# Kernel tuning notes

Measured on AMD Instinct MI355X. Metric: run time of the kernel, lower is better.

Reference implementation:

```python
import jax, jax.numpy as jnp
import numpy as np

D_MODEL = 1024
N_HEADS = 16
D_K = D_MODEL // N_HEADS


def setup_inputs() -> dict:
    key = jax.random.key(0)
    ks = jax.random.split(key, 9)
    B, S = 2, 2048
    scale = 1.0 / np.sqrt(D_MODEL)
    inp = {
        "X": jax.random.normal(ks[0], (B, S, D_MODEL), dtype=jnp.float32),
        "Wq": jax.random.normal(ks[1], (D_MODEL, D_MODEL), dtype=jnp.float32) * scale,
        "bq": jnp.zeros((D_MODEL,), dtype=jnp.float32),
        "Wk": jax.random.normal(ks[2], (D_MODEL, D_MODEL), dtype=jnp.float32) * scale,
        "bk": jnp.zeros((D_MODEL,), dtype=jnp.float32),
        "Wv": jax.random.normal(ks[3], (D_MODEL, D_MODEL), dtype=jnp.float32) * scale,
        "bv": jnp.zeros((D_MODEL,), dtype=jnp.float32),
        "Wo": jax.random.normal(ks[4], (D_MODEL, D_MODEL), dtype=jnp.float32) * scale,
        "bo": jnp.zeros((D_MODEL,), dtype=jnp.float32),
    }
    return inp


def reference(X, Wq, bq, Wk, bk, Wv, bv, Wo, bo):
    B, S, _ = X.shape
    # QKV projections (torch Linear: x @ W.T + b; here W stored as [in, out])
    Q = X @ Wq + bq
    K = X @ Wk + bk
    V = X @ Wv + bv
    # [B, S, H, Dk] -> [B, H, S, Dk]
    def split_heads(t):
        return t.reshape(B, S, N_HEADS, D_K).transpose(0, 2, 1, 3)
    Q, K, V = split_heads(Q), split_heads(K), split_heads(V)
    scores = jnp.einsum('bhqd,bhkd->bhqk', Q, K) / jnp.sqrt(jnp.float32(D_K))
    attn = jax.nn.softmax(scores, axis=-1)
    out = jnp.einsum('bhqk,bhkd->bhqd', attn, V)  # [B, H, S, Dk]
    out = out.transpose(0, 2, 1, 3).reshape(B, S, D_MODEL)
    return out @ Wo + bo
```

## Files before the change

### kernel.cpp

```cpp
#include <hip/hip_runtime.h>
#include <hip/hip_bf16.h>


typedef __attribute__((ext_vector_type(8))) short short8;
typedef __attribute__((ext_vector_type(4))) float f32x4;
typedef __attribute__((ext_vector_type(2))) float f32x2;
typedef unsigned short u16;
typedef unsigned int u32;

static __device__ __forceinline__ u16 f2bf(float f) {
    union { float f; u32 u; } c; c.f = f;
    u32 u = c.u;
    u32 r = u + 0x7fffu + ((u >> 16) & 1u);
    return (u16)(r >> 16);
}
static __device__ __forceinline__ float bf2f(u16 x) {
    union { u32 u; float f; } c; c.u = ((u32)x) << 16;
    return c.f;
}

#define GL1(p) ((const __attribute__((address_space(1))) void*)(p))
#define LD3(p) ((__attribute__((address_space(3))) void*)(p))
static __device__ __forceinline__ void gld16(const void* g, void* l) {
    __builtin_amdgcn_global_load_lds(GL1(g), LD3(l), 16, 0, 0);
}

#define Q_PRESCALE 0.18033688011112042f

__global__ __launch_bounds__(256) void prep(
    const float* __restrict__ X, u16* __restrict__ Xb,
    const float* __restrict__ Wq, const float* __restrict__ Wk,
    const float* __restrict__ Wv, const float* __restrict__ Wo,
    const float* __restrict__ bq, const float* __restrict__ bk,
    const float* __restrict__ bv,
    u16* __restrict__ Wqkv, u16* __restrict__ Wto, float* __restrict__ Bp)
{
    int id = blockIdx.x;
    int t = threadIdx.x;
    if (id == 5120) {
        for (int i = t; i < 3072; i += 256) {
            int wsel = i >> 10, c = i & 1023;
            float v = (wsel == 0) ? bq[c] * Q_PRESCALE : (wsel == 1 ? bk[c] : bv[c]);
            Bp[i] = v;
        }
        return;
    }
    if (id >= 1024) {
        int i = (id - 1024) * 1024 + t * 4;
        float4 v = *reinterpret_cast<const float4*>(X + i);
        ushort4 o;
        o.x = f2bf(v.x); o.y = f2bf(v.y); o.z = f2bf(v.z); o.w = f2bf(v.w);
        *reinterpret_cast<ushort4*>(Xb + i) = o;
        return;
    }
    int which = id >> 8;
    const float* W; u16* T; float sc;
    switch (which) {
        case 0: W = Wq; T = Wqkv;                sc = Q_PRESCALE; break;
        case 1: W = Wk; T = Wqkv + 1024 * 1024;  sc = 1.0f; break;
        case 2: W = Wv; T = Wqkv + 2048 * 1024;  sc = 1.0f; break;
        default: W = Wo; T = Wto;                sc = 1.0f; break;
    }
    int rem = id & 255;
    int n0 = (rem & 15) * 64, k0 = (rem >> 4) * 64;
    __shared__ float tile[64][65];
    int r = t / 16, c4 = (t % 16) * 4;
    #pragma unroll
    for (int p = 0; p < 4; p++) {
        int row = p * 16 + r;
        float4 v = *reinterpret_cast<const float4*>(W + (k0 + row) * 1024 + n0 + c4);
        tile[row][c4 + 0] = v.x * sc; tile[row][c4 + 1] = v.y * sc;
        tile[row][c4 + 2] = v.z * sc; tile[row][c4 + 3] = v.w * sc;
    }
    __syncthreads();
    #pragma unroll
    for (int p = 0; p < 4; p++) {
        int nrow = p * 16 + r;
        ushort4 o;
        o.x = f2bf(tile[c4 + 0][nrow]); o.y = f2bf(tile[c4 + 1][nrow]);
        o.z = f2bf(tile[c4 + 2][nrow]); o.w = f2bf(tile[c4 + 3][nrow]);
        *reinterpret_cast<ushort4*>(T + (n0 + nrow) * 1024 + k0 + c4) = o;
    }
}

__global__ __launch_bounds__(256, 3) void gemm_qkv(
    const u16* __restrict__ Xb, const u16* __restrict__ Wqkv,
    const float* __restrict__ Bp,
    u16* __restrict__ Qb, u16* __restrict__ Kb, u16* __restrict__ Vtg)
{
    __shared__ __align__(16) u16 As[2][128 * 32];
    __shared__ __align__(16) u16 Bs[2][128 * 32];
    int t = threadIdx.x;
    int w = t >> 6, lane = t & 63, l15 = lane & 15, quad = lane >> 4;
    int wm = (w >> 1) * 64, wn = (w & 1) * 64;
    int bid = blockIdx.x;
    int row0 = (bid & 31) * 128, col0 = (bid >> 5) * 128;

    int drow = lane >> 2;
    int gc8 = ((lane & 3) ^ (drow & 3) ^ ((drow >> 2) & 3)) * 8;
    int asw = ((quad ^ (l15 & 3) ^ ((l15 >> 2) & 3)) & 3) * 8;

    const u16* Ag = Xb + (row0 + drow) * 1024 + gc8;
    const u16* Bg = Wqkv + (col0 + drow) * 1024 + gc8;

    f32x4 acc[4][4];
    #pragma unroll
    for (int i = 0; i < 4; i++)
        #pragma unroll
        for (int j = 0; j < 4; j++)
            acc[i][j] = (f32x4){0.f, 0.f, 0.f, 0.f};

    #pragma unroll
    for (int q = 0; q < 2; q++) {
        int rr = w * 32 + q * 16;
        gld16(Ag + rr * 1024, &As[0][rr * 32]);
        gld16(Bg + rr * 1024, &Bs[0][rr * 32]);
    }
    for (int kt = 0; kt < 32; kt++) {
        __syncthreads();
        int cur = kt & 1;
        if (kt < 31) {
            int k0 = (kt + 1) * 32;
            #pragma unroll
            for (int q = 0; q < 2; q++) {
                int rr = w * 32 + q * 16;
                gld16(Ag + rr * 1024 + k0, &As[cur ^ 1][rr * 32]);
                gld16(Bg + rr * 1024 + k0, &Bs[cur ^ 1][rr * 32]);
            }
        }
        short8 a[4], b[4];
        #pragma unroll
        for (int i = 0; i < 4; i++)
            a[i] = *reinterpret_cast<const short8*>(&As[cur][(wm + i * 16 + l15) * 32 + asw]);
        #pragma unroll
        for (int j = 0; j < 4; j++)
            b[j] = *reinterpret_cast<const short8*>(&Bs[cur][(wn + j * 16 + l15) * 32 + asw]);
        #pragma unroll
        for (int i = 0; i < 4; i++)
            #pragma unroll
            for (int j = 0; j < 4; j++)
                acc[i][j] = __builtin_amdgcn_mfma_f32_16x16x32_bf16(a[i], b[j], acc[i][j], 0, 0, 0);
    }

    int osel = col0 >> 10;
    if (osel == 2) {
        #pragma unroll
        for (int i = 0; i < 4; i++) {
            int gr = row0 + wm + i * 16 + quad * 4;
            int b_ = gr >> 11, s = gr & 2047;
            #pragma unroll
            for (int j = 0; j < 4; j++) {
                int col = col0 + wn + j * 16 + l15;
                int c = col & 1023, h = c >> 6, d = c & 63;
                float bb = Bp[col];
                ushort4 pk;
                pk.x = f2bf(acc[i][j][0] + bb);
                pk.y = f2bf(acc[i][j][1] + bb);
                pk.z = f2bf(acc[i][j][2] + bb);
                pk.w = f2bf(acc[i][j][3] + bb);
                *reinterpret_cast<ushort4*>(&Vtg[((b_ * 16 + h) * 64 + d) * 2048 + s]) = pk;
            }
        }
    } else {
        u16* dst = osel ? Kb : Qb;
        #pragma unroll
        for (int i = 0; i < 4; i++) {
            int rowb = row0 + wm + i * 16 + quad * 4;
            #pragma unroll
            for (int j = 0; j < 4; j++) {
                int col = col0 + wn + j * 16 + l15;
                int c = col & 1023, h = c >> 6, d = c & 63;
                float bb = Bp[col];
                #pragma unroll
                for (int r = 0; r < 4; r++) {
                    int gr = rowb + r;
                    int b_ = gr >> 11, s = gr & 2047;
                    dst[(((b_ << 4) + h) * 2048 + s) * 64 + d] = f2bf(acc[i][j][r] + bb);
                }
            }
        }
    }
}

__global__ __launch_bounds__(256) void attn(
    const u16* __restrict__ Qb, const u16* __restrict__ Kb,
    const u16* __restrict__ Vtg, u16* __restrict__ Opart, float* __restrict__ Lsum)
{
    int bid = blockIdx.x;
    int bh = bid & 31, sp = (bid >> 5) & 3, qt = bid >> 7;
    int b_ = bh >> 4, h = bh & 15;
    const u16* Qp = Qb + bh * (2048 * 64);
    const u16* Kp = Kb + bh * (2048 * 64);
    const u16* Vp = Vtg + bh * (64 * 2048);
    u16* Op = Opart + sp * (4096 * 1024);
    float* Lp = Lsum + sp * (32 * 2048) + bh * 2048;

    __shared__ __align__(16) u16 Ks[64 * 64];
    __shared__ __align__(16) u16 Vt[64 * 64];
    __shared__ __align__(16) u16 Ps[128 * 64];

    int t = threadIdx.x, w = t >> 6, lane = t & 63, l15 = lane & 15, quad = lane >> 4;

    short8 qf[2][2];
    #pragma unroll
    for (int f = 0; f < 2; f++)
        #pragma unroll
        for (int ds = 0; ds < 2; ds++)
            qf[f][ds] = *reinterpret_cast<const short8*>(
                &Qp[(qt * 128 + w * 32 + f * 16 + l15) * 64 + ds * 32 + quad * 8]);

    int di = lane >> 3;
    int dc8 = ((lane & 7) ^ di) * 8;

    int rl = l15 & 7, rh = l15 >> 3;
    int koff[4][2];
    #pragma unroll
    for (int j = 0; j < 4; j++)
        #pragma unroll
        for (int ds = 0; ds < 2; ds++)
            koff[j][ds] = (j * 2 + rh) * 512 + rl * 64 + (((ds * 4 + quad) ^ rl) & 7) * 8;

    int pwt[2][4];
    #pragma unroll
    for (int f = 0; f < 2; f++)
        #pragma unroll
        for (int j = 0; j < 4; j++)
            pwt[f][j] = (w * 32 + f * 16 + l15) * 64 +
                        (((2 * j + (quad >> 1)) ^ rl) * 8) + (quad & 1) * 4;
    int prt[2][2];
    #pragma unroll
    for (int f = 0; f < 2; f++)
        #pragma unroll
        for (int ks = 0; ks < 2; ks++)
            prt[f][ks] = (w * 32 + f * 16 + l15) * 64 + (((4 * ks + quad) ^ rl) * 8);

    f32x4 acc[2][4];
    f32x2 lsum2[2] = {(f32x2){0.f, 0.f}, (f32x2){0.f, 0.f}};
    #pragma unroll
    for (int f = 0; f < 2; f++)
        #pragma unroll
        for (int j = 0; j < 4; j++) acc[f][j] = (f32x4){0.f, 0.f, 0.f, 0.f};

    int kb0 = sp * 512;
    for (int kt = 0; kt < 8; kt++) {
        int kbase = kb0 + kt * 64;
        __syncthreads();
        #pragma unroll
        for (int sg = 0; sg < 2; sg++) {
            int seg = w * 2 + sg;
            gld16(&Kp[(kbase + seg * 8 + di) * 64 + dc8], &Ks[seg * 512]);
            gld16(&Vp[(seg * 8 + di) * 2048 + kbase + dc8], &Vt[seg * 512]);
        }
        __syncthreads();

        f32x4 sc[2][4];
        #pragma unroll
        for (int j = 0; j < 4; j++) {
            f32x4 s0 = (f32x4){0.f, 0.f, 0.f, 0.f};
            f32x4 s1 = (f32x4){0.f, 0.f, 0.f, 0.f};
            #pragma unroll
            for (int ds = 0; ds < 2; ds++) {
                short8 kf = *reinterpret_cast<const short8*>(&Ks[koff[j][ds]]);
                s0 = __builtin_amdgcn_mfma_f32_16x16x32_bf16(kf, qf[0][ds], s0, 0, 0, 0);
                s1 = __builtin_amdgcn_mfma_f32_16x16x32_bf16(kf, qf[1][ds], s1, 0, 0, 0);
            }
            sc[0][j] = s0; sc[1][j] = s1;
        }

        #pragma unroll
        for (int f = 0; f < 2; f++)
            #pragma unroll
            for (int j = 0; j < 4; j++) {
                float p0 = __builtin_amdgcn_exp2f(sc[f][j][0]);
                float p1 = __builtin_amdgcn_exp2f(sc[f][j][1]);
                float p2 = __builtin_amdgcn_exp2f(sc[f][j][2]);
                float p3 = __builtin_amdgcn_exp2f(sc[f][j][3]);
                lsum2[f] += (f32x2){p0, p1};
                lsum2[f] += (f32x2){p2, p3};
                union { float fv; u32 uv; } c0, c1, c2, c3;
                c0.fv = p0; c1.fv = p1; c2.fv = p2; c3.fv = p3;
                uint2 pk;
                pk.x = (c0.uv >> 16) | (c1.uv & 0xffff0000u);
                pk.y = (c2.uv >> 16) | (c3.uv & 0xffff0000u);
                *reinterpret_cast<uint2*>(&Ps[pwt[f][j]]) = pk;
            }

        #pragma unroll
        for (int ks = 0; ks < 2; ks++) {
            short8 pf0 = *reinterpret_cast<const short8*>(&Ps[prt[0][ks]]);
            short8 pf1 = *reinterpret_cast<const short8*>(&Ps[prt[1][ks]]);
            #pragma unroll
            for (int j = 0; j < 4; j++) {
                short8 vf = *reinterpret_cast<const short8*>(&Vt[koff[j][ks]]);
                acc[0][j] = __builtin_amdgcn_mfma_f32_16x16x32_bf16(pf0, vf, acc[0][j], 0, 0, 0);
                acc[1][j] = __builtin_amdgcn_mfma_f32_16x16x32_bf16(pf1, vf, acc[1][j], 0, 0, 0);
            }
        }
    }

    #pragma unroll
    for (int f = 0; f < 2; f++) {
        float s = lsum2[f].x + lsum2[f].y;
        s += __shfl_xor(s, 16);
        s += __shfl_xor(s, 32);
        if (quad == 0)
            Lp[qt * 128 + w * 32 + f * 16 + l15] = s;
    }

    #pragma unroll
    for (int f = 0; f < 2; f++)
        #pragma unroll
        for (int j = 0; j < 4; j++)
            #pragma unroll
            for (int r = 0; r < 4; r++) {
                int srow = qt * 128 + w * 32 + f * 16 + quad * 4 + r;
                Op[(b_ * 2048 + srow) * 1024 + h * 64 + j * 16 + l15] = f2bf(acc[f][j][r]);
            }
}

__global__ __launch_bounds__(256) void combine(
    const u16* __restrict__ Op, const float* __restrict__ Ls,
    u16* __restrict__ Ob)
{
    int idx8 = (blockIdx.x * 256 + threadIdx.x) * 8;
    int row = idx8 >> 10, col = idx8 & 1023;
    int b_ = row >> 11, s = row & 2047, h = col >> 6;
    int li = (b_ * 16 + h) * 2048 + s;
    float l = Ls[li] + Ls[li + 65536] + Ls[li + 131072] + Ls[li + 196608];
    float inv = 1.0f / l;
    float accv[8];
    #pragma unroll
    for (int i = 0; i < 8; i++) accv[i] = 0.f;
    #pragma unroll
    for (int p = 0; p < 4; p++) {
        union { uint4 v; u16 s[8]; } ua;
        ua.v = *reinterpret_cast<const uint4*>(&Op[p * 4194304 + idx8]);
        #pragma unroll
        for (int i = 0; i < 8; i++) accv[i] += bf2f(ua.s[i]);
    }
    union { uint4 v; u16 s[8]; } uo;
    #pragma unroll
    for (int i = 0; i < 8; i++) uo.s[i] = f2bf(accv[i] * inv);
    *reinterpret_cast<uint4*>(&Ob[idx8]) = uo.v;
}

__global__ __launch_bounds__(256, 3) void gemm_out(
    const u16* __restrict__ Ob, const u16* __restrict__ Wto,
    const float* __restrict__ bo, float* __restrict__ out)
{
    __shared__ __align__(16) u16 As[2][128 * 32];
    __shared__ __align__(16) u16 Bs[2][128 * 32];
    int t = threadIdx.x;
    int w = t >> 6, lane = t & 63, l15 = lane & 15, quad = lane >> 4;
    int wm = (w >> 1) * 64, wn = (w & 1) * 64;
    int bid = blockIdx.x;
    int row0 = (bid & 31) * 128, col0 = (bid >> 5) * 128;

    int drow = lane >> 2;
    int gc8 = ((lane & 3) ^ (drow & 3) ^ ((drow >> 2) & 3)) * 8;
    int asw = ((quad ^ (l15 & 3) ^ ((l15 >> 2) & 3)) & 3) * 8;

    const u16* Ag = Ob + (row0 + drow) * 1024 + gc8;
    const u16* Bg = Wto + (col0 + drow) * 1024 + gc8;

    f32x4 acc[4][4];
    #pragma unroll
    for (int i = 0; i < 4; i++)
        #pragma unroll
        for (int j = 0; j < 4; j++)
            acc[i][j] = (f32x4){0.f, 0.f, 0.f, 0.f};

    #pragma unroll
    for (int q = 0; q < 2; q++) {
        int rr = w * 32 + q * 16;
        gld16(Ag + rr * 1024, &As[0][rr * 32]);
        gld16(Bg + rr * 1024, &Bs[0][rr * 32]);
    }
    for (int kt = 0; kt < 32; kt++) {
        __syncthreads();
        int cur = kt & 1;
        if (kt < 31) {
            int k0 = (kt + 1) * 32;
            #pragma unroll
            for (int q = 0; q < 2; q++) {
                int rr = w * 32 + q * 16;
                gld16(Ag + rr * 1024 + k0, &As[cur ^ 1][rr * 32]);
                gld16(Bg + rr * 1024 + k0, &Bs[cur ^ 1][rr * 32]);
            }
        }
        short8 a[4], b[4];
        #pragma unroll
        for (int i = 0; i < 4; i++)
            a[i] = *reinterpret_cast<const short8*>(&As[cur][(wm + i * 16 + l15) * 32 + asw]);
        #pragma unroll
        for (int j = 0; j < 4; j++)
            b[j] = *reinterpret_cast<const short8*>(&Bs[cur][(wn + j * 16 + l15) * 32 + asw]);
        #pragma unroll
        for (int i = 0; i < 4; i++)
            #pragma unroll
            for (int j = 0; j < 4; j++)
                acc[i][j] = __builtin_amdgcn_mfma_f32_16x16x32_bf16(a[i], b[j], acc[i][j], 0, 0, 0);
    }
    #pragma unroll
    for (int i = 0; i < 4; i++) {
        int rowb = row0 + wm + i * 16 + quad * 4;
        #pragma unroll
        for (int j = 0; j < 4; j++) {
            int col = col0 + wn + j * 16 + l15;
            float bb = bo[col];
            #pragma unroll
            for (int r = 0; r < 4; r++)
                out[(rowb + r) * 1024 + col] = acc[i][j][r] + bb;
        }
    }
}

extern "C" void kernel_launch(void* const* d_in, const int* in_sizes, int n_in,
                              void* d_out, int out_size, void* d_ws, size_t ws_size,
                              hipStream_t stream) {
    const float* X  = (const float*)d_in[0];
    const float* Wq = (const float*)d_in[1];
    const float* bq = (const float*)d_in[2];
    const float* Wk = (const float*)d_in[3];
    const float* bk = (const float*)d_in[4];
    const float* Wv = (const float*)d_in[5];
    const float* bv = (const float*)d_in[6];
    const float* Wo = (const float*)d_in[7];
    const float* bo = (const float*)d_in[8];
    float* out = (float*)d_out;

    char* ws = (char*)d_ws;
    u16* Xb    = (u16*)(ws);
    u16* Ob    = (u16*)(ws);
    u16* Wqkv  = (u16*)(ws + (8u  << 20));
    u16* Wto   = (u16*)(ws + (14u << 20));
    float* Bp  = (float*)(ws + (16u << 20));
    u16* Qb    = (u16*)(ws + (17u << 20));
    u16* Kb    = (u16*)(ws + (25u << 20));
    u16* Vtg   = (u16*)(ws + (33u << 20));
    u16* Op    = (u16*)(ws + (41u << 20));
    float* Ls  = (float*)(ws + (73u << 20));

    prep     <<<5121, 256, 0, stream>>>(X, Xb, Wq, Wk, Wv, Wo, bq, bk, bv, Wqkv, Wto, Bp);
    gemm_qkv <<<768, 256, 0, stream>>>(Xb, Wqkv, Bp, Qb, Kb, Vtg);
    attn     <<<2048, 256, 0, stream>>>(Qb, Kb, Vtg, Op, Ls);
    combine  <<<2048, 256, 0, stream>>>(Op, Ls, Ob);
    gemm_out <<<256, 256, 0, stream>>>(Ob, Wto, bo, out);
}
```

Before: 205.1 us.

## Fuse split-K combine into attention tail and shrink GEMM tiles for occupancy

```diff
diff --git a/kernel.cpp b/kernel.cpp
--- a/kernel.cpp
+++ b/kernel.cpp
@@ -33,7 +33,8 @@
     const float* __restrict__ Wv, const float* __restrict__ Wo,
     const float* __restrict__ bq, const float* __restrict__ bk,
     const float* __restrict__ bv,
-    u16* __restrict__ Wqkv, u16* __restrict__ Wto, float* __restrict__ Bp)
+    u16* __restrict__ Wqkv, u16* __restrict__ Wto, float* __restrict__ Bp,
+    u32* __restrict__ Fl)
 {
     int id = blockIdx.x;
     int t = threadIdx.x;
@@ -43,6 +44,7 @@
             float v = (wsel == 0) ? bq[c] * Q_PRESCALE : (wsel == 1 ? bk[c] : bv[c]);
             Bp[i] = v;
         }
+        for (int i = t; i < 512; i += 256) Fl[i] = 0u;
         return;
     }
     if (id >= 1024) {
@@ -83,18 +85,18 @@
     }
 }
 
-__global__ __launch_bounds__(256, 3) void gemm_qkv(
+__global__ __launch_bounds__(256, 4) void gemm_qkv(
     const u16* __restrict__ Xb, const u16* __restrict__ Wqkv,
     const float* __restrict__ Bp,
     u16* __restrict__ Qb, u16* __restrict__ Kb, u16* __restrict__ Vtg)
 {
-    __shared__ __align__(16) u16 As[2][128 * 32];
+    __shared__ __align__(16) u16 As[2][64 * 32];
     __shared__ __align__(16) u16 Bs[2][128 * 32];
     int t = threadIdx.x;
     int w = t >> 6, lane = t & 63, l15 = lane & 15, quad = lane >> 4;
-    int wm = (w >> 1) * 64, wn = (w & 1) * 64;
+    int wm = (w >> 1) * 32, wn = (w & 1) * 64;
     int bid = blockIdx.x;
-    int row0 = (bid & 31) * 128, col0 = (bid >> 5) * 128;
+    int row0 = (bid & 63) * 64, col0 = (bid >> 6) * 128;
 
     int drow = lane >> 2;
     int gc8 = ((lane & 3) ^ (drow & 3) ^ ((drow >> 2) & 3)) * 8;
@@ -103,40 +105,37 @@
     const u16* Ag = Xb + (row0 + drow) * 1024 + gc8;
     const u16* Bg = Wqkv + (col0 + drow) * 1024 + gc8;
 
-    f32x4 acc[4][4];
-    #pragma unroll
-    for (int i = 0; i < 4; i++)
+    f32x4 acc[2][4];
+    #pragma unroll
+    for (int i = 0; i < 2; i++)
         #pragma unroll
         for (int j = 0; j < 4; j++)
             acc[i][j] = (f32x4){0.f, 0.f, 0.f, 0.f};
 
-    #pragma unroll
-    for (int q = 0; q < 2; q++) {
-        int rr = w * 32 + q * 16;
-        gld16(Ag + rr * 1024, &As[0][rr * 32]);
-        gld16(Bg + rr * 1024, &Bs[0][rr * 32]);
-    }
+    gld16(Ag + (w * 16) * 1024, &As[0][(w * 16) * 32]);
+    #pragma unroll
+    for (int q = 0; q < 2; q++)
+        gld16(Bg + (w * 32 + q * 16) * 1024, &Bs[0][(w * 32 + q * 16) * 32]);
+
     for (int kt = 0; kt < 32; kt++) {
         __syncthreads();
         int cur = kt & 1;
         if (kt < 31) {
             int k0 = (kt + 1) * 32;
-            #pragma unroll
-            for (int q = 0; q < 2; q++) {
-                int rr = w * 32 + q * 16;
-                gld16(Ag + rr * 1024 + k0, &As[cur ^ 1][rr * 32]);
-                gld16(Bg + rr * 1024 + k0, &Bs[cur ^ 1][rr * 32]);
-            }
-        }
-        short8 a[4], b[4];
-        #pragma unroll
-        for (int i = 0; i < 4; i++)
+            gld16(Ag + (w * 16) * 1024 + k0, &As[cur ^ 1][(w * 16) * 32]);
+            #pragma unroll
+            for (int q = 0; q < 2; q++)
+                gld16(Bg + (w * 32 + q * 16) * 1024 + k0, &Bs[cur ^ 1][(w * 32 + q * 16) * 32]);
+        }
+        short8 a[2], b[4];
+        #pragma unroll
+        for (int i = 0; i < 2; i++)
             a[i] = *reinterpret_cast<const short8*>(&As[cur][(wm + i * 16 + l15) * 32 + asw]);
         #pragma unroll
         for (int j = 0; j < 4; j++)
             b[j] = *reinterpret_cast<const short8*>(&Bs[cur][(wn + j * 16 + l15) * 32 + asw]);
         #pragma unroll
-        for (int i = 0; i < 4; i++)
+        for (int i = 0; i < 2; i++)
             #pragma unroll
             for (int j = 0; j < 4; j++)
                 acc[i][j] = __builtin_amdgcn_mfma_f32_16x16x32_bf16(a[i], b[j], acc[i][j], 0, 0, 0);
@@ -145,7 +144,7 @@
     int osel = col0 >> 10;
     if (osel == 2) {
         #pragma unroll
-        for (int i = 0; i < 4; i++) {
+        for (int i = 0; i < 2; i++) {
             int gr = row0 + wm + i * 16 + quad * 4;
             int b_ = gr >> 11, s = gr & 2047;
             #pragma unroll
@@ -164,7 +163,7 @@
     } else {
         u16* dst = osel ? Kb : Qb;
         #pragma unroll
-        for (int i = 0; i < 4; i++) {
+        for (int i = 0; i < 2; i++) {
             int rowb = row0 + wm + i * 16 + quad * 4;
             #pragma unroll
             for (int j = 0; j < 4; j++) {
@@ -184,7 +183,8 @@
 
 __global__ __launch_bounds__(256) void attn(
     const u16* __restrict__ Qb, const u16* __restrict__ Kb,
-    const u16* __restrict__ Vtg, u16* __restrict__ Opart, float* __restrict__ Lsum)
+    const u16* __restrict__ Vtg, u16* __restrict__ Opart, float* __restrict__ Lsum,
+    u32* __restrict__ Fl, u16* __restrict__ Ob)
 {
     int bid = blockIdx.x;
     int bh = bid & 31, sp = (bid >> 5) & 3, qt = bid >> 7;
@@ -198,6 +198,7 @@
     __shared__ __align__(16) u16 Ks[64 * 64];
     __shared__ __align__(16) u16 Vt[64 * 64];
     __shared__ __align__(16) u16 Ps[128 * 64];
+    __shared__ u32 s_old;
 
     int t = threadIdx.x, w = t >> 6, lane = t & 63, l15 = lane & 15, quad = lane >> 4;
 
@@ -316,45 +317,52 @@
                 int srow = qt * 128 + w * 32 + f * 16 + quad * 4 + r;
                 Op[(b_ * 2048 + srow) * 1024 + h * 64 + j * 16 + l15] = f2bf(acc[f][j][r]);
             }
-}
-
-__global__ __launch_bounds__(256) void combine(
-    const u16* __restrict__ Op, const float* __restrict__ Ls,
-    u16* __restrict__ Ob)
-{
-    int idx8 = (blockIdx.x * 256 + threadIdx.x) * 8;
-    int row = idx8 >> 10, col = idx8 & 1023;
-    int b_ = row >> 11, s = row & 2047, h = col >> 6;
-    int li = (b_ * 16 + h) * 2048 + s;
-    float l = Ls[li] + Ls[li + 65536] + Ls[li + 131072] + Ls[li + 196608];
-    float inv = 1.0f / l;
-    float accv[8];
-    #pragma unroll
-    for (int i = 0; i < 8; i++) accv[i] = 0.f;
-    #pragma unroll
-    for (int p = 0; p < 4; p++) {
-        union { uint4 v; u16 s[8]; } ua;
-        ua.v = *reinterpret_cast<const uint4*>(&Op[p * 4194304 + idx8]);
-        #pragma unroll
-        for (int i = 0; i < 8; i++) accv[i] += bf2f(ua.s[i]);
-    }
-    union { uint4 v; u16 s[8]; } uo;
-    #pragma unroll
-    for (int i = 0; i < 8; i++) uo.s[i] = f2bf(accv[i] * inv);
-    *reinterpret_cast<uint4*>(&Ob[idx8]) = uo.v;
-}
-
-__global__ __launch_bounds__(256, 3) void gemm_out(
+
+    __threadfence();
+    __syncthreads();
+    if (t == 0) s_old = atomicAdd(&Fl[qt * 32 + bh], 1u);
+    __syncthreads();
+    if (s_old == 3u) {
+        __threadfence();
+        int row = t >> 1;
+        int cbase = (t & 1) * 32;
+        int srow = qt * 128 + row;
+        float l = Lsum[bh * 2048 + srow] + Lsum[65536 + bh * 2048 + srow] +
+                  Lsum[131072 + bh * 2048 + srow] + Lsum[196608 + bh * 2048 + srow];
+        float inv = 1.0f / l;
+        int off0 = (b_ * 2048 + srow) * 1024 + h * 64 + cbase;
+        #pragma unroll
+        for (int cc = 0; cc < 4; cc++) {
+            int off = off0 + cc * 8;
+            float accv[8];
+            #pragma unroll
+            for (int i = 0; i < 8; i++) accv[i] = 0.f;
+            #pragma unroll
+            for (int p = 0; p < 4; p++) {
+                union { uint4 v; u16 s[8]; } ua;
+                ua.v = *reinterpret_cast<const uint4*>(&Opart[p * 4194304 + off]);
+                #pragma unroll
+                for (int i = 0; i < 8; i++) accv[i] += bf2f(ua.s[i]);
+            }
+            union { uint4 v; u16 s[8]; } uo;
+            #pragma unroll
+            for (int i = 0; i < 8; i++) uo.s[i] = f2bf(accv[i] * inv);
+            *reinterpret_cast<uint4*>(&Ob[off]) = uo.v;
+        }
+    }
+}
+
+__global__ __launch_bounds__(256, 4) void gemm_out(
     const u16* __restrict__ Ob, const u16* __restrict__ Wto,
     const float* __restrict__ bo, float* __restrict__ out)
 {
     __shared__ __align__(16) u16 As[2][128 * 32];
-    __shared__ __align__(16) u16 Bs[2][128 * 32];
+    __shared__ __align__(16) u16 Bs[2][64 * 32];
     int t = threadIdx.x;
     int w = t >> 6, lane = t & 63, l15 = lane & 15, quad = lane >> 4;
-    int wm = (w >> 1) * 64, wn = (w & 1) * 64;
+    int wm = (w >> 1) * 64, wn = (w & 1) * 32;
     int bid = blockIdx.x;
-    int row0 = (bid & 31) * 128, col0 = (bid >> 5) * 128;
+    int row0 = (bid & 31) * 128, col0 = (bid >> 5) * 64;
 
     int drow = lane >> 2;
     int gc8 = ((lane & 3) ^ (drow & 3) ^ ((drow >> 2) & 3)) * 8;
@@ -363,49 +371,46 @@
     const u16* Ag = Ob + (row0 + drow) * 1024 + gc8;
     const u16* Bg = Wto + (col0 + drow) * 1024 + gc8;
 
-    f32x4 acc[4][4];
+    f32x4 acc[4][2];
     #pragma unroll
     for (int i = 0; i < 4; i++)
         #pragma unroll
-        for (int j = 0; j < 4; j++)
+        for (int j = 0; j < 2; j++)
             acc[i][j] = (f32x4){0.f, 0.f, 0.f, 0.f};
 
     #pragma unroll
-    for (int q = 0; q < 2; q++) {
-        int rr = w * 32 + q * 16;
-        gld16(Ag + rr * 1024, &As[0][rr * 32]);
-        gld16(Bg + rr * 1024, &Bs[0][rr * 32]);
-    }
+    for (int q = 0; q < 2; q++)
+        gld16(Ag + (w * 32 + q * 16) * 1024, &As[0][(w * 32 + q * 16) * 32]);
+    gld16(Bg + (w * 16) * 1024, &Bs[0][(w * 16) * 32]);
+
     for (int kt = 0; kt < 32; kt++) {
         __syncthreads();
         int cur = kt & 1;
         if (kt < 31) {
             int k0 = (kt + 1) * 32;
             #pragma unroll
-            for (int q = 0; q < 2; q++) {
-                int rr = w * 32 + q * 16;
-                gld16(Ag + rr * 1024 + k0, &As[cur ^ 1][rr * 32]);
-                gld16(Bg + rr * 1024 + k0, &Bs[cur ^ 1][rr * 32]);
-            }
-        }
-        short8 a[4], b[4];
+            for (int q = 0; q < 2; q++)
+                gld16(Ag + (w * 32 + q * 16) * 1024 + k0, &As[cur ^ 1][(w * 32 + q * 16) * 32]);
+            gld16(Bg + (w * 16) * 1024 + k0, &Bs[cur ^ 1][(w * 16) * 32]);
+        }
+        short8 a[4], b[2];
         #pragma unroll
         for (int i = 0; i < 4; i++)
             a[i] = *reinterpret_cast<const short8*>(&As[cur][(wm + i * 16 + l15) * 32 + asw]);
         #pragma unroll
-        for (int j = 0; j < 4; j++)
+        for (int j = 0; j < 2; j++)
             b[j] = *reinterpret_cast<const short8*>(&Bs[cur][(wn + j * 16 + l15) * 32 + asw]);
         #pragma unroll
         for (int i = 0; i < 4; i++)
             #pragma unroll
-            for (int j = 0; j < 4; j++)
+            for (int j = 0; j < 2; j++)
                 acc[i][j] = __builtin_amdgcn_mfma_f32_16x16x32_bf16(a[i], b[j], acc[i][j], 0, 0, 0);
     }
     #pragma unroll
     for (int i = 0; i < 4; i++) {
         int rowb = row0 + wm + i * 16 + quad * 4;
         #pragma unroll
-        for (int j = 0; j < 4; j++) {
+        for (int j = 0; j < 2; j++) {
             int col = col0 + wn + j * 16 + l15;
             float bb = bo[col];
             #pragma unroll
@@ -440,10 +445,10 @@
     u16* Vtg   = (u16*)(ws + (33u << 20));
     u16* Op    = (u16*)(ws + (41u << 20));
     float* Ls  = (float*)(ws + (73u << 20));
-
-    prep     <<<5121, 256, 0, stream>>>(X, Xb, Wq, Wk, Wv, Wo, bq, bk, bv, Wqkv, Wto, Bp);
-    gemm_qkv <<<768, 256, 0, stream>>>(Xb, Wqkv, Bp, Qb, Kb, Vtg);
-    attn     <<<2048, 256, 0, stream>>>(Qb, Kb, Vtg, Op, Ls);
-    combine  <<<2048, 256, 0, stream>>>(Op, Ls, Ob);
-    gemm_out <<<256, 256, 0, stream>>>(Ob, Wto, bo, out);
-}
+    u32* Fl    = (u32*)(ws + (74u << 20));
+
+    prep     <<<5121, 256, 0, stream>>>(X, Xb, Wq, Wk, Wv, Wo, bq, bk, bv, Wqkv, Wto, Bp, Fl);
+    gemm_qkv <<<1536, 256, 0, stream>>>(Xb, Wqkv, Bp, Qb, Kb, Vtg);
+    attn     <<<2048, 256, 0, stream>>>(Qb, Kb, Vtg, Op, Ls, Fl, Ob);
+    gemm_out <<<512, 256, 0, stream>>>(Ob, Wto, bo, out);
+}
```

Result: slower. 558.2 us (+172.2%).
